# Kernel tuning notes

Measured on AMD Instinct MI355X. Metric: run time of the kernel, lower is better.

Reference implementation:

```python
import jax, jax.numpy as jnp
import numpy as np

B, T, D = 2, 2048, 2048
NH, HD = 16, 128
Q_LAT, KV_LAT = 1024, 512
EPS = 1e-6
THETA = 10000.0


def setup_inputs() -> dict:
    key = jax.random.key(0)
    ks = jax.random.split(key, 8)
    x = jax.random.normal(ks[0], (B, T, D), dtype=jnp.float32)
    # causal additive mask, broadcast over batch/heads
    neg = jnp.finfo(jnp.float32).min
    causal = jnp.where(jnp.tril(jnp.ones((T, T), dtype=bool)), 0.0, neg)
    attn_mask = causal[None, None, :, :].astype(jnp.float32)
    s = lambda fan_in: 1.0 / np.sqrt(fan_in)
    q_a_w = jax.random.normal(ks[1], (Q_LAT, D), dtype=jnp.float32) * s(D)
    q_b_w = jax.random.normal(ks[2], (NH * HD, Q_LAT), dtype=jnp.float32) * s(Q_LAT)
    kv_a_w = jax.random.normal(ks[3], (KV_LAT, D), dtype=jnp.float32) * s(D)
    k_b_w = jax.random.normal(ks[4], (NH * HD, KV_LAT), dtype=jnp.float32) * s(KV_LAT)
    v_b_w = jax.random.normal(ks[5], (NH * HD, KV_LAT), dtype=jnp.float32) * s(KV_LAT)
    o_w = jax.random.normal(ks[6], (D, NH * HD), dtype=jnp.float32) * s(NH * HD)
    q_norm_w = jnp.ones((HD,), dtype=jnp.float32)
    k_norm_w = jnp.ones((HD,), dtype=jnp.float32)
    return dict(x=x, attn_mask=attn_mask, q_a_w=q_a_w, q_b_w=q_b_w, kv_a_w=kv_a_w,
                k_b_w=k_b_w, v_b_w=v_b_w, o_w=o_w, q_norm_w=q_norm_w, k_norm_w=k_norm_w)


def _rms_norm(x, w):
    var = jnp.mean(jnp.square(x), axis=-1, keepdims=True)
    return x * jax.lax.rsqrt(var + EPS) * w


def _rope_cache(t, hd, dtype):
    inv_freq = 1.0 / (THETA ** (jnp.arange(0, hd, 2, dtype=jnp.float32) / hd))
    freqs = jnp.arange(t, dtype=jnp.float32)[:, None] * inv_freq[None, :]  # [t, hd/2]
    emb = jnp.concatenate([freqs, freqs], axis=-1)  # [t, hd]
    return jnp.cos(emb).astype(dtype), jnp.sin(emb).astype(dtype)


def _rotate_half(x):
    h = x.shape[-1] // 2
    return jnp.concatenate([-x[..., h:], x[..., :h]], axis=-1)


def reference(x, attn_mask, q_a_w, q_b_w, kv_a_w, k_b_w, v_b_w, o_w, q_norm_w, k_norm_w):
    b, t, d = x.shape
    # low-rank projections (torch Linear: y = x @ W.T)
    q = (x @ q_a_w.T) @ q_b_w.T          # [b, t, nh*hd]
    kv = x @ kv_a_w.T                     # [b, t, kv_lat]
    k = kv @ k_b_w.T
    v = kv @ v_b_w.T
    q = q.reshape(b, t, NH, HD).transpose(0, 2, 1, 3)  # [b, nh, t, hd]
    k = k.reshape(b, t, NH, HD).transpose(0, 2, 1, 3)
    v = v.reshape(b, t, NH, HD).transpose(0, 2, 1, 3)
    # QK-norm over head dim
    q = _rms_norm(q, q_norm_w)
    k = _rms_norm(k, k_norm_w)
    # RoPE
    cos, sin = _rope_cache(t, HD, x.dtype)  # [t, hd]
    cos = cos[None, None, :, :]
    sin = sin[None, None, :, :]
    q = q * cos + _rotate_half(q) * sin
    k = k * cos + _rotate_half(k) * sin
    # attention
    sd = 1.0 / np.sqrt(HD)
    attn = jnp.einsum('bhqd,bhkd->bhqk', q, k) * sd + attn_mask
    attn = jax.nn.softmax(attn, axis=-1)
    out = jnp.einsum('bhqk,bhkd->bhqd', attn, v)
    out = out.transpose(0, 2, 1, 3).reshape(b, t, NH * HD)
    return out @ o_w.T
```

## Files before the change

kernel.cpp:

```cpp
#include <hip/hip_runtime.h>
#include <hip/hip_fp16.h>

typedef _Float16 f16;
typedef _Float16 f16x4 __attribute__((ext_vector_type(4)));
typedef _Float16 f16x8 __attribute__((ext_vector_type(8)));
typedef float f32x4 __attribute__((ext_vector_type(4)));

#define BT 4096
#define DMODEL 2048

__device__ __forceinline__ void gld16(const f16* g, f16* l) {
    __builtin_amdgcn_global_load_lds((const __attribute__((address_space(1))) void*)g,
                                     (__attribute__((address_space(3))) void*)l, 16, 0, 0);
}

struct Cvt7 {
    const float* s[7];
    f16* d[7];
    int off4[8];
};
__global__ __launch_bounds__(256) void k_cvt7(Cvt7 c) {
    int i = blockIdx.x * 256 + threadIdx.x;
    if (i >= c.off4[7]) return;
    int seg = 0;
#pragma unroll
    for (int k = 1; k < 7; ++k) seg += (i >= c.off4[k]);
    int j = i - c.off4[seg];
    float4 v = ((const float4*)c.s[seg])[j];
    f16x4 h;
    h[0] = (f16)v.x; h[1] = (f16)v.y; h[2] = (f16)v.z; h[3] = (f16)v.w;
    ((f16x4*)c.d[seg])[j] = h;
}

template <int MODE, typename CT>
__global__ __launch_bounds__(512, 2) void k_gemm8(const f16* __restrict__ A,
                                                  const f16* __restrict__ B0,
                                                  const f16* __restrict__ B1,
                                                  CT* __restrict__ C0,
                                                  f16* __restrict__ C1,
                                                  int K, int nsplit, int ld0, int ld1) {
    __shared__ __align__(16) f16 lds[49152];
    const int tid = threadIdx.x;
    const int w = tid >> 6, l = tid & 63;
    const int wm = w >> 2, wn = w & 3;
    const int quad = l >> 4, ln = l & 15;
    const int gx = gridDim.x;
    const int lin = blockIdx.y * gx + blockIdx.x;
    const int nwg = gx << 5;
    const int chunk = (lin & 7) * (nwg >> 3) + (lin >> 3);
    const int m0 = (chunk & 31) * 128, n0 = (chunk >> 5) * 256;

    const f16* Bp;
    if constexpr (MODE == 0) {
        Bp = B0 + (size_t)n0 * K;
    } else if constexpr (MODE == 1) {
        Bp = (n0 < nsplit) ? B0 + (size_t)n0 * K : B1 + (size_t)(n0 - nsplit) * K;
    } else {
        Bp = (n0 < 2048) ? B0 + (size_t)n0 * K : B1 + (size_t)(n0 - 2048) * K;
    }

    const f16* ag  = A + (size_t)(m0 + w * 16 + (l >> 2)) * K + (l & 3) * 8;
    const f16* bg0 = Bp + (size_t)(w * 16 + (l >> 2)) * K + (l & 3) * 8;
    const f16* bg1 = bg0 + (size_t)128 * K;
    f16* al = &lds[w * 512];
    f16* bl = &lds[4096 + w * 512];

#define STAGE8(buf_, kc_, t_)                          \
    {                                                  \
        const int off_ = ((buf_) * 2 + (kc_)) * 12288; \
        const int g_ = (t_) * 64 + (kc_) * 32;         \
        gld16(ag + g_, al + off_);                     \
        gld16(bg0 + g_, bl + off_);                    \
        gld16(bg1 + g_, bl + off_ + 4096);             \
    }

    f32x4 acc[4][4];
#pragma unroll
    for (int i = 0; i < 4; ++i)
#pragma unroll
        for (int j = 0; j < 4; ++j)
#pragma unroll
            for (int r = 0; r < 4; ++r) acc[i][j][r] = 0.f;

    const int nt = K >> 6;
    STAGE8(0, 0, 0);
    STAGE8(0, 1, 0);
    STAGE8(1, 0, 1);
    asm volatile("s_waitcnt vmcnt(3)" ::: "memory");
    __builtin_amdgcn_s_barrier();
    asm volatile("s_waitcnt lgkmcnt(0)" ::: "memory");

    for (int t = 0; t < nt; ++t) {
        const int buf = t & 1;
#pragma unroll
        for (int kc = 0; kc < 2; ++kc) {
            const f16* Ah = &lds[(buf * 2 + kc) * 12288];
            const f16* Bh = Ah + 4096;
            f16x8 a[4], b[4];
#pragma unroll
            for (int i = 0; i < 4; ++i)
                a[i] = *(const f16x8*)&Ah[(wm * 64 + i * 16 + ln) * 32 + quad * 8];
#pragma unroll
            for (int j = 0; j < 4; ++j)
                b[j] = *(const f16x8*)&Bh[(wn * 64 + j * 16 + ln) * 32 + quad * 8];
            if (kc == 0) {
                if (t + 1 < nt) STAGE8(buf ^ 1, 1, t + 1);
            } else {
                if (t + 2 < nt) STAGE8(buf, 0, t + 2);
            }
            __builtin_amdgcn_s_barrier();
            asm volatile("s_waitcnt lgkmcnt(0)" ::: "memory");
            __builtin_amdgcn_s_setprio(1);
#pragma unroll
            for (int i = 0; i < 4; ++i)
#pragma unroll
                for (int j = 0; j < 4; ++j)
                    acc[i][j] = __builtin_amdgcn_mfma_f32_16x16x32_f16(a[i], b[j], acc[i][j], 0, 0, 0);
            __builtin_amdgcn_s_setprio(0);
            if (kc == 1 && t + 1 < nt) {
                if (t + 2 < nt) asm volatile("s_waitcnt vmcnt(3)" ::: "memory");
                else            asm volatile("s_waitcnt vmcnt(0)" ::: "memory");
            }
            __builtin_amdgcn_s_barrier();
        }
    }
#undef STAGE8

    if constexpr (MODE == 2) {
        if (n0 >= 2048) {
            const int d0 = n0 - 2048;
            const int bb = m0 >> 11, tb = m0 & 2047;
#pragma unroll
            for (int i = 0; i < 4; ++i)
#pragma unroll
                for (int j = 0; j < 4; ++j) {
                    f16x4 v;
#pragma unroll
                    for (int r = 0; r < 4; ++r) v[r] = (f16)acc[i][j][r];
                    *(f16x4*)&C1[((size_t)(bb * 2048 + d0 + wn * 64 + j * 16 + ln)) * 2048 +
                                 tb + wm * 64 + i * 16 + quad * 4] = v;
                }
            return;
        }
    }

    CT* Cd; int ldc; int cb;
    if constexpr (MODE == 0) {
        Cd = C0; ldc = ld0; cb = n0;
    } else if constexpr (MODE == 1) {
        if (n0 < nsplit) { Cd = C0; ldc = ld0; cb = n0; }
        else             { Cd = (CT*)C1; ldc = ld1; cb = n0 - nsplit; }
    } else {
        Cd = C0; ldc = 2048; cb = n0;
    }

    const int p = (wm ? 16 : 0) + quad * 4;
    if constexpr (sizeof(CT) == 2) {
        f16* Cs = (f16*)lds;
#pragma unroll
        for (int i = 0; i < 4; ++i) {
            __syncthreads();
#pragma unroll
            for (int j = 0; j < 4; ++j)
#pragma unroll
                for (int r = 0; r < 4; ++r)
                    Cs[(p + r) * 264 + wn * 64 + j * 16 + ln] = (f16)acc[i][j][r];
            __syncthreads();
#pragma unroll
            for (int rr = 0; rr < 2; ++rr) {
                int idx = rr * 512 + tid;
                int row = idx >> 5, c8 = idx & 31;
                int rg = m0 + i * 16 + (row & 15) + ((row & 16) ? 64 : 0);
                *(f16x8*)&Cd[(size_t)rg * ldc + cb + c8 * 8] = *(const f16x8*)&Cs[row * 264 + c8 * 8];
            }
        }
    } else {
        float* Cs = (float*)lds;
#pragma unroll
        for (int i = 0; i < 4; ++i) {
            __syncthreads();
#pragma unroll
            for (int j = 0; j < 4; ++j)
#pragma unroll
                for (int r = 0; r < 4; ++r)
                    Cs[(p + r) * 260 + wn * 64 + j * 16 + ln] = acc[i][j][r];
            __syncthreads();
#pragma unroll
            for (int rr = 0; rr < 4; ++rr) {
                int idx = rr * 512 + tid;
                int row = idx >> 6, c4 = idx & 63;
                int rg = m0 + i * 16 + (row & 15) + ((row & 16) ? 64 : 0);
                *(float4*)&Cd[(size_t)rg * ldc + cb + c4 * 4] = *(const float4*)&Cs[row * 260 + c4 * 4];
            }
        }
    }
}

__global__ __launch_bounds__(256) void k_norm_rope(f16* __restrict__ q, f16* __restrict__ k,
                                                   const float* __restrict__ qw,
                                                   const float* __restrict__ kw) {
    const int gw = blockIdx.x * 4 + (threadIdx.x >> 6);
    const int l = threadIdx.x & 63;
    const int which = gw >> 16;
    const int rh = gw & 65535;
    const int row = rh >> 4, h = rh & 15;
    f16* p = which ? k : q;
    const float* wp = which ? kw : qw;
    const float scale = which ? 1.0f : 0.08838834764831843f;
    const size_t base = (size_t)row * DMODEL + h * 128;
    float xa = (float)p[base + l];
    float xb = (float)p[base + 64 + l];
    float ss = xa * xa + xb * xb;
#pragma unroll
    for (int off = 32; off > 0; off >>= 1) ss += __shfl_xor(ss, off);
    const float rms = rsqrtf(ss * (1.0f / 128.0f) + 1e-6f);
    const float na = xa * rms * wp[l];
    const float nb = xb * rms * wp[64 + l];
    const int t = row & 2047;
    const float freq = __expf((float)l * -0.1439115683121279f);
    const float ang = (float)t * freq;
    const float c = cosf(ang), s = sinf(ang);
    p[base + l]      = (f16)((na * c - nb * s) * scale);
    p[base + 64 + l] = (f16)((nb * c + na * s) * scale);
}

__global__ __launch_bounds__(256, 3) void k_flash(const f16* __restrict__ Q, const f16* __restrict__ K,
                                                  const f16* __restrict__ Vt, f16* __restrict__ O) {
    __shared__ f16 Kl[64 * 136];
    __shared__ f16 Vl[128 * 72];
    const int h = blockIdx.x, b = blockIdx.y, mt = 31 - blockIdx.z;
    const int tid = threadIdx.x, w = tid >> 6, l64 = tid & 63;
    const int quad = l64 >> 4, ln = l64 & 15;

    f16x8 qf[4];
    {
        const int tq = mt * 64 + w * 16 + ln;
        const f16* qp = Q + (size_t)(b * 2048 + tq) * DMODEL + h * 128 + quad * 8;
#pragma unroll
        for (int kc = 0; kc < 4; ++kc) qf[kc] = *(const f16x8*)(qp + kc * 32);
    }
    f32x4 oacc[8];
#pragma unroll
    for (int ot = 0; ot < 8; ++ot)
#pragma unroll
        for (int r = 0; r < 4; ++r) oacc[ot][r] = 0.f;
    float m_r = -INFINITY, l_r = 0.f;

    const f16* kbase = K + (size_t)(b * 2048) * DMODEL + h * 128;
    const f16* vbase = Vt + (size_t)(b * 2048 + h * 128) * 2048;

    f16x8 kr[4], vr[4];
#pragma unroll
    for (int c = 0; c < 4; ++c) {
        int idx = c * 256 + tid;
        kr[c] = *(const f16x8*)(kbase + (size_t)(idx >> 4) * DMODEL + (idx & 15) * 8);
        vr[c] = *(const f16x8*)(vbase + (size_t)(idx >> 3) * 2048 + (idx & 7) * 8);
    }

    for (int j = 0; j <= mt; ++j) {
        __syncthreads();
#pragma unroll
        for (int c = 0; c < 4; ++c) {
            int idx = c * 256 + tid;
            *(f16x8*)&Kl[(idx >> 4) * 136 + (idx & 15) * 8] = kr[c];
            *(f16x8*)&Vl[(idx >> 3) * 72 + (idx & 7) * 8] = vr[c];
        }
        __syncthreads();
        if (j < mt) {
#pragma unroll
            for (int c = 0; c < 4; ++c) {
                int idx = c * 256 + tid;
                kr[c] = *(const f16x8*)(kbase + (size_t)((j + 1) * 64 + (idx >> 4)) * DMODEL + (idx & 15) * 8);
                vr[c] = *(const f16x8*)(vbase + (size_t)(idx >> 3) * 2048 + (j + 1) * 64 + (idx & 7) * 8);
            }
        }
        f32x4 sacc[4];
#pragma unroll
        for (int nt = 0; nt < 4; ++nt)
#pragma unroll
            for (int r = 0; r < 4; ++r) sacc[nt][r] = 0.f;
#pragma unroll
        for (int nt = 0; nt < 4; ++nt)
#pragma unroll
            for (int kc = 0; kc < 4; ++kc) {
                f16x8 kf = *(const f16x8*)&Kl[(nt * 16 + ln) * 136 + kc * 32 + quad * 8];
                sacc[nt] = __builtin_amdgcn_mfma_f32_16x16x32_f16(kf, qf[kc], sacc[nt], 0, 0, 0);
            }
        if (j == mt) {
#pragma unroll
            for (int nt = 0; nt < 4; ++nt)
#pragma unroll
                for (int r = 0; r < 4; ++r)
                    if (nt * 16 + quad * 4 + r > w * 16 + ln) sacc[nt][r] = -INFINITY;
        }
        float mx = -INFINITY;
#pragma unroll
        for (int nt = 0; nt < 4; ++nt)
#pragma unroll
            for (int r = 0; r < 4; ++r) mx = fmaxf(mx, sacc[nt][r]);
        mx = fmaxf(mx, __shfl_xor(mx, 16));
        mx = fmaxf(mx, __shfl_xor(mx, 32));
        const bool grow = (mx > m_r + 8.f);
        const float mn = grow ? fmaxf(m_r, mx) : m_r;
        const float alpha = grow ? __expf(m_r - mn) : 1.f;
        m_r = mn;
        f16x4 pa[4];
        float s0 = 0.f;
#pragma unroll
        for (int nt = 0; nt < 4; ++nt)
#pragma unroll
            for (int r = 0; r < 4; ++r) {
                float pv = __expf(sacc[nt][r] - mn);
                s0 += pv;
                pa[nt][r] = (f16)pv;
            }
        s0 += __shfl_xor(s0, 16);
        s0 += __shfl_xor(s0, 32);
        l_r = l_r * alpha + s0;
        if (__ballot(grow)) {
            float ar[4];
#pragma unroll
            for (int r = 0; r < 4; ++r) ar[r] = __shfl(alpha, (l64 & 48) | (quad * 4 + r));
#pragma unroll
            for (int ot = 0; ot < 8; ++ot)
#pragma unroll
                for (int r = 0; r < 4; ++r) oacc[ot][r] *= ar[r];
        }
#pragma unroll
        for (int nt = 0; nt < 4; ++nt)
#pragma unroll
            for (int ot = 0; ot < 8; ++ot) {
                f16x4 vf = *(const f16x4*)&Vl[(ot * 16 + ln) * 72 + nt * 16 + quad * 4];
                oacc[ot] = __builtin_amdgcn_mfma_f32_16x16x16f16(pa[nt], vf, oacc[ot], 0, 0, 0);
            }
    }
    const float inv = 1.0f / l_r;
    float ivr[4];
#pragma unroll
    for (int r = 0; r < 4; ++r) ivr[r] = __shfl(inv, (l64 & 48) | (quad * 4 + r));
    __syncthreads();
#pragma unroll
    for (int ot = 0; ot < 8; ++ot)
#pragma unroll
        for (int r = 0; r < 4; ++r)
            Kl[(w * 16 + quad * 4 + r) * 136 + ot * 16 + ln] = (f16)(oacc[ot][r] * ivr[r]);
    __syncthreads();
#pragma unroll
    for (int c = 0; c < 4; ++c) {
        int idx = c * 256 + tid;
        int row = idx >> 4, col8 = (idx & 15) * 8;
        *(f16x8*)&O[(size_t)(b * 2048 + mt * 64 + row) * DMODEL + h * 128 + col8] =
            *(const f16x8*)&Kl[row * 136 + col8];
    }
}

extern "C" void kernel_launch(void* const* d_in, const int* in_sizes, int n_in,
                              void* d_out, int out_size, void* d_ws, size_t ws_size,
                              hipStream_t stream) {
    const float* x    = (const float*)d_in[0];
    const float* qaw  = (const float*)d_in[2];
    const float* qbw  = (const float*)d_in[3];
    const float* kvaw = (const float*)d_in[4];
    const float* kbw  = (const float*)d_in[5];
    const float* vbw  = (const float*)d_in[6];
    const float* ow   = (const float*)d_in[7];
    const float* qnw  = (const float*)d_in[8];
    const float* knw  = (const float*)d_in[9];
    float* out = (float*)d_out;

    char* p = (char*)d_ws;
    auto alloc = [&](size_t elems) { f16* r = (f16*)p; p += elems * sizeof(f16); return r; };
    f16* xb   = alloc((size_t)BT * 2048);
    f16* wo   = alloc((size_t)2048 * 2048);
    f16* wqa  = alloc((size_t)1024 * 2048);
    f16* wqb  = alloc((size_t)2048 * 1024);
    f16* wkva = alloc((size_t)512 * 2048);
    f16* wkb  = alloc((size_t)2048 * 512);
    f16* wvb  = alloc((size_t)2048 * 512);
    f16* qlat = alloc((size_t)BT * 1024);
    f16* kvb  = alloc((size_t)BT * 512);
    f16* qpre = alloc((size_t)BT * 2048);
    f16* kpre = alloc((size_t)BT * 2048);
    f16* vt   = xb;
    f16* attn = wqa;

    Cvt7 c;
    c.s[0] = x;    c.d[0] = xb;
    c.s[1] = qaw;  c.d[1] = wqa;
    c.s[2] = qbw;  c.d[2] = wqb;
    c.s[3] = kvaw; c.d[3] = wkva;
    c.s[4] = kbw;  c.d[4] = wkb;
    c.s[5] = vbw;  c.d[5] = wvb;
    c.s[6] = ow;   c.d[6] = wo;
    int sz4[7] = {BT * 2048 / 4, 1024 * 2048 / 4, 2048 * 1024 / 4, 512 * 2048 / 4,
                  2048 * 512 / 4, 2048 * 512 / 4, 2048 * 2048 / 4};
    c.off4[0] = 0;
    for (int i = 0; i < 7; ++i) c.off4[i + 1] = c.off4[i] + sz4[i];
    k_cvt7<<<(c.off4[7] + 255) / 256, 256, 0, stream>>>(c);

    k_gemm8<1, f16><<<dim3(1536 / 256, BT / 128), 512, 0, stream>>>(
        xb, wqa, wkva, qlat, kvb, 2048, 1024, 1024, 512);
    k_gemm8<0, f16><<<dim3(2048 / 256, BT / 128), 512, 0, stream>>>(
        qlat, wqb, nullptr, qpre, nullptr, 1024, 0, 2048, 0);
    k_gemm8<2, f16><<<dim3(4096 / 256, BT / 128), 512, 0, stream>>>(
        kvb, wkb, wvb, kpre, vt, 512, 0, 0, 0);
    k_norm_rope<<<32768, 256, 0, stream>>>(qpre, kpre, qnw, knw);
    k_flash<<<dim3(16, 2, 32), 256, 0, stream>>>(qpre, kpre, vt, attn);
    k_gemm8<0, float><<<dim3(2048 / 256, BT / 128), 512, 0, stream>>>(
        attn, wo, nullptr, out, nullptr, 2048, 0, 2048, 0);
}
```

Before: 381.5 us.

## Fuse QK RMS-norm and RoPE into the Q/K projection GEMM epilogue

Removes the standalone norm+rope kernel and applies RMS normalization, rotary embedding and the softmax scale inside the f16 store epilogue of the Q-up and K-up GEMMs. The per-head sum of squares is reduced with lane shuffles across the 16 lanes that hold one 128-wide head row, and the rotate-half partner comes from a shuffle with lane offset 8. This avoids a full extra read and write pass over the Q and K activations plus one kernel launch. In exchange, the GEMM epilogue does more transcendental math and shuffles, and the fused path relies on the store layout mapping each 16-lane group to exactly one head row.

New measurement: 447.8 us. 1.17x slower.

```diff
diff --git a/kernel.cpp b/kernel.cpp
--- a/kernel.cpp
+++ b/kernel.cpp
@@ -32,12 +32,13 @@
     ((f16x4*)c.d[seg])[j] = h;
 }
 
-template <int MODE, typename CT>
+template <int MODE, int FUSE, typename CT>
 __global__ __launch_bounds__(512, 2) void k_gemm8(const f16* __restrict__ A,
                                                   const f16* __restrict__ B0,
                                                   const f16* __restrict__ B1,
                                                   CT* __restrict__ C0,
                                                   f16* __restrict__ C1,
+                                                  const float* __restrict__ nw,
                                                   int K, int nsplit, int ld0, int ld1) {
     __shared__ __align__(16) f16 lds[49152];
     const int tid = threadIdx.x;
@@ -171,7 +172,35 @@
                 int idx = rr * 512 + tid;
                 int row = idx >> 5, c8 = idx & 31;
                 int rg = m0 + i * 16 + (row & 15) + ((row & 16) ? 64 : 0);
-                *(f16x8*)&Cd[(size_t)rg * ldc + cb + c8 * 8] = *(const f16x8*)&Cs[row * 264 + c8 * 8];
+                f16x8 v = *(const f16x8*)&Cs[row * 264 + c8 * 8];
+                if constexpr (FUSE != 0) {
+                    float x[8];
+                    float ss = 0.f;
+#pragma unroll
+                    for (int k = 0; k < 8; ++k) { x[k] = (float)v[k]; ss += x[k] * x[k]; }
+                    ss += __shfl_xor(ss, 1);
+                    ss += __shfl_xor(ss, 2);
+                    ss += __shfl_xor(ss, 4);
+                    ss += __shfl_xor(ss, 8);
+                    const float rms = rsqrtf(ss * (1.0f / 128.0f) + 1e-6f);
+                    const int hc = c8 & 15;
+                    const int tt = rg & 2047;
+                    float nv[8];
+#pragma unroll
+                    for (int k = 0; k < 8; ++k) nv[k] = x[k] * rms * nw[hc * 8 + k];
+                    float pv[8];
+#pragma unroll
+                    for (int k = 0; k < 8; ++k) pv[k] = __shfl_xor(nv[k], 8);
+                    const float sgn = (hc >= 8) ? 1.f : -1.f;
+                    const float scale = (FUSE == 1) ? 0.08838834764831843f : 1.0f;
+#pragma unroll
+                    for (int k = 0; k < 8; ++k) {
+                        const int d = (hc & 7) * 8 + k;
+                        const float ang = (float)tt * __expf((float)d * -0.1439115683121279f);
+                        v[k] = (f16)((nv[k] * cosf(ang) + sgn * pv[k] * sinf(ang)) * scale);
+                    }
+                }
+                *(f16x8*)&Cd[(size_t)rg * ldc + cb + c8 * 8] = v;
             }
         }
     } else {
@@ -194,34 +223,6 @@
             }
         }
     }
-}
-
-__global__ __launch_bounds__(256) void k_norm_rope(f16* __restrict__ q, f16* __restrict__ k,
-                                                   const float* __restrict__ qw,
-                                                   const float* __restrict__ kw) {
-    const int gw = blockIdx.x * 4 + (threadIdx.x >> 6);
-    const int l = threadIdx.x & 63;
-    const int which = gw >> 16;
-    const int rh = gw & 65535;
-    const int row = rh >> 4, h = rh & 15;
-    f16* p = which ? k : q;
-    const float* wp = which ? kw : qw;
-    const float scale = which ? 1.0f : 0.08838834764831843f;
-    const size_t base = (size_t)row * DMODEL + h * 128;
-    float xa = (float)p[base + l];
-    float xb = (float)p[base + 64 + l];
-    float ss = xa * xa + xb * xb;
-#pragma unroll
-    for (int off = 32; off > 0; off >>= 1) ss += __shfl_xor(ss, off);
-    const float rms = rsqrtf(ss * (1.0f / 128.0f) + 1e-6f);
-    const float na = xa * rms * wp[l];
-    const float nb = xb * rms * wp[64 + l];
-    const int t = row & 2047;
-    const float freq = __expf((float)l * -0.1439115683121279f);
-    const float ang = (float)t * freq;
-    const float c = cosf(ang), s = sinf(ang);
-    p[base + l]      = (f16)((na * c - nb * s) * scale);
-    p[base + 64 + l] = (f16)((nb * c + na * s) * scale);
 }
 
 __global__ __launch_bounds__(256, 3) void k_flash(const f16* __restrict__ Q, const f16* __restrict__ K,
@@ -398,14 +399,13 @@
     for (int i = 0; i < 7; ++i) c.off4[i + 1] = c.off4[i] + sz4[i];
     k_cvt7<<<(c.off4[7] + 255) / 256, 256, 0, stream>>>(c);
 
-    k_gemm8<1, f16><<<dim3(1536 / 256, BT / 128), 512, 0, stream>>>(
-        xb, wqa, wkva, qlat, kvb, 2048, 1024, 1024, 512);
-    k_gemm8<0, f16><<<dim3(2048 / 256, BT / 128), 512, 0, stream>>>(
-        qlat, wqb, nullptr, qpre, nullptr, 1024, 0, 2048, 0);
-    k_gemm8<2, f16><<<dim3(4096 / 256, BT / 128), 512, 0, stream>>>(
-        kvb, wkb, wvb, kpre, vt, 512, 0, 0, 0);
-    k_norm_rope<<<32768, 256, 0, stream>>>(qpre, kpre, qnw, knw);
+    k_gemm8<1, 0, f16><<<dim3(1536 / 256, BT / 128), 512, 0, stream>>>(
+        xb, wqa, wkva, qlat, kvb, nullptr, 2048, 1024, 1024, 512);
+    k_gemm8<0, 1, f16><<<dim3(2048 / 256, BT / 128), 512, 0, stream>>>(
+        qlat, wqb, nullptr, qpre, nullptr, qnw, 1024, 0, 2048, 0);
+    k_gemm8<2, 2, f16><<<dim3(4096 / 256, BT / 128), 512, 0, stream>>>(
+        kvb, wkb, wvb, kpre, vt, knw, 512, 0, 0, 0);
     k_flash<<<dim3(16, 2, 32), 256, 0, stream>>>(qpre, kpre, vt, attn);
-    k_gemm8<0, float><<<dim3(2048 / 256, BT / 128), 512, 0, stream>>>(
-        attn, wo, nullptr, out, nullptr, 2048, 0, 2048, 0);
+    k_gemm8<0, 0, float><<<dim3(2048 / 256, BT / 128), 512, 0, stream>>>(
+        attn, wo, nullptr, out, nullptr, nullptr, 2048, 0, 2048, 0);
 }
```
